# Kernel optimization log

Hardware: AMD Instinct MI355X
Metric: run time of the kernel (lower is better)

Reference implementation:

```python
import jax, jax.numpy as jnp
import numpy as np

L = 18                      # tree depth, N = 2**L - 1 nodes (complete binary tree)
N = 2**L - 1               # 262143
D = 128                     # embedding dim
V = 100000                  # vocab size of the single data type
E = 8                       # edge_count


def setup_inputs() -> dict:
    key = jax.random.key(0)
    ks = jax.random.split(key, 8)
    data = jax.random.randint(ks[0], (N,), 0, V)
    edges = jax.random.randint(ks[1], (N,), 0, E)
    data_vecs = jax.random.normal(ks[2], (V, D), dtype=jnp.float32) * 0.1
    # torch uses torch.rand (U[0,1)); scaled for numerical stability over 18 levels
    data_W = jax.random.uniform(ks[3], (D, D), dtype=jnp.float32) * 0.1
    data_b = jax.random.uniform(ks[4], (D,), dtype=jnp.float32) * 0.1
    edge_W = jax.random.uniform(ks[5], (E, D, D), dtype=jnp.float32) * (2.0 / D)
    edge_b = jax.random.uniform(ks[6], (E, D), dtype=jnp.float32) * 0.1
    score_W = jax.random.uniform(ks[7], (D, 1), dtype=jnp.float32)
    return {"data": data, "edges": edges, "data_vecs": data_vecs,
            "data_W": data_W, "data_b": data_b, "edge_W": edge_W,
            "edge_b": edge_b, "score_W": score_W}


def reference(data, edges, data_vecs, data_W, data_b, edge_W, edge_b, score_W):
    # per-node leaf term: addmm(data_bias, data_vecs[data], data_W)  -> [N, D]
    raw = data_vecs[data] @ data_W + data_b
    ret = raw    # value returned to the parent (leaves: unclamped)
    emb = raw    # stored embedding (internal nodes: pre-clamp h)
    # bottom-up over levels; level l occupies indices [2**l - 1, 2**(l+1) - 1)
    for l in reversed(range(L - 1)):
        p0, npar = 2**l - 1, 2**l
        c0, M = 2**(l + 1) - 1, 2**(l + 1)
        child_ret = ret[c0:c0 + M]              # [M, D], siblings adjacent
        eids = edges[c0:c0 + M]                 # [M]
        # edge-weighted child transform: child @ edge_W[e] + edge_b[e]
        contrib = edge_b[eids]
        for e in range(E):                      # small static edge loop
            contrib = contrib + jnp.where((eids == e)[:, None], child_ret, 0.0) @ edge_W[e]
        # sum the two children of each parent, then (leaf + children) / (nc + 1)
        contrib = contrib.reshape(npar, 2, D).sum(axis=1)
        h = (raw[p0:p0 + npar] + contrib) / 3.0
        emb = emb.at[p0:p0 + npar].set(h)
        ret = ret.at[p0:p0 + npar].set(jnp.maximum(h, 0.0))
    scores = (emb @ score_W)[:, 0]              # [N]
    return scores


if __name__ == "__main__":
    out = reference(**setup_inputs())
    print(out.shape, out.dtype)
```

## Files before the change

kernel.cpp:

```cpp
#include <hip/hip_runtime.h>

#define D 128
#define NLVL 17
#define TS 128
#define LVLPAD 1024
#define LDSTR 136
#define LEAF_BLKS 1032
#define CHUNK 2048
#define CNT_BLKS 128

typedef float  floatx4 __attribute__((ext_vector_type(4)));
typedef short  shortx8 __attribute__((ext_vector_type(8)));

__device__ __forceinline__ unsigned short f2bf(float f) {
    unsigned u = __float_as_uint(f);
    u += 0x7FFFu + ((u >> 16) & 1u);
    return (unsigned short)(u >> 16);
}
__device__ __forceinline__ float bf2f(unsigned short h) {
    return __uint_as_float(((unsigned)h) << 16);
}
__device__ __forceinline__ int lvl_base_dev(int l) { return ((2 << l) - 2) + LVLPAD * l; }

__global__ __launch_bounds__(256) void prep_kernel(
    const float* __restrict__ dW, const float* __restrict__ db,
    const float* __restrict__ eW, const float* __restrict__ eb,
    const float* __restrict__ sWs, const float* __restrict__ vecs,
    const int* __restrict__ edges,
    unsigned short* __restrict__ ewt, unsigned short* __restrict__ cwt,
    unsigned short* __restrict__ dwt, float* __restrict__ dcomp,
    float* __restrict__ sv, float* __restrict__ s0, int* __restrict__ ctr,
    int* __restrict__ gcnt128, int Nn,
    unsigned short* __restrict__ vbf, int n4)
{
    __shared__ float smem[8448];
    const int b = blockIdx.x, t = threadIdx.x;
    if (b < 32) {
        float* w_s = smem;
        float* cs  = smem + 4096;
        const int e = b >> 2, cc = b & 3;
        for (int i = t; i < D * 8; i += 256) {
            const int k = i >> 3, j4 = i & 7;
            ((float4*)w_s)[i] = ((const float4*)eW)[((size_t)e * D + k) * 32 + cc * 8 + j4];
        }
        __syncthreads();
        const int r2 = t >> 1, h = t & 1;
        float4 acc[4];
        #pragma unroll
        for (int m = 0; m < 4; m++) acc[m] = make_float4(0.f, 0.f, 0.f, 0.f);
        for (int k = 0; k < D; k++) {
            const float a = dW[(size_t)r2 * D + k];
            #pragma unroll
            for (int m = 0; m < 4; m++) {
                const float4 w4 = ((const float4*)w_s)[k * 8 + h * 4 + m];
                acc[m].x += a * w4.x; acc[m].y += a * w4.y; acc[m].z += a * w4.z; acc[m].w += a * w4.w;
            }
        }
        #pragma unroll
        for (int m = 0; m < 4; m++) {
            cs[r2 * 33 + h * 16 + m * 4 + 0] = acc[m].x;
            cs[r2 * 33 + h * 16 + m * 4 + 1] = acc[m].y;
            cs[r2 * 33 + h * 16 + m * 4 + 2] = acc[m].z;
            cs[r2 * 33 + h * 16 + m * 4 + 3] = acc[m].w;
        }
        __syncthreads();
        {
            const int nn = t >> 3, kseg = t & 7, k0 = kseg * 16;
            unsigned ow[8];
            #pragma unroll
            for (int i2 = 0; i2 < 8; i2++) {
                const unsigned short lo = f2bf(cs[(k0 + 2 * i2) * 33 + nn]);
                const unsigned short hi = f2bf(cs[(k0 + 2 * i2 + 1) * 33 + nn]);
                ow[i2] = (unsigned)lo | ((unsigned)hi << 16);
            }
            uint4* dstp = (uint4*)(cwt + (size_t)e * D * D + (size_t)(cc * 32 + nn) * D + k0);
            dstp[0] = make_uint4(ow[0], ow[1], ow[2], ow[3]);
            dstp[1] = make_uint4(ow[4], ow[5], ow[6], ow[7]);
        }
        if (t < 32) {
            float a2 = 0.f;
            for (int k = 0; k < D; k++) a2 += db[k] * w_s[k * 32 + t];
            dcomp[e * D + cc * 32 + t] = a2 + eb[e * D + cc * 32 + t];
        }
    } else if (b < 41) {
        float* lds = smem;
        const int bb = b - 32;
        const float* src = (bb < 8) ? (eW + (size_t)bb * D * D) : dW;
        unsigned short* dst = (bb < 8) ? (ewt + (size_t)bb * D * D) : dwt;
        for (int half = 0; half < 2; half++) {
            __syncthreads();
            for (int i = t; i < 64 * D / 4; i += 256) {
                float4 v = ((const float4*)src)[half * (64 * D / 4) + i];
                const int k = (i * 4) >> 7, n = (i * 4) & 127;
                lds[k * 129 + n]     = v.x;
                lds[k * 129 + n + 1] = v.y;
                lds[k * 129 + n + 2] = v.z;
                lds[k * 129 + n + 3] = v.w;
            }
            __syncthreads();
            const int n = t >> 1, hh = t & 1;
            for (int kk = 0; kk < 32; kk++) {
                const int k = hh * 32 + kk;
                dst[(size_t)n * D + half * 64 + k] = f2bf(lds[k * 129 + n]);
            }
        }
    } else if (b == 41) {
        float* red = smem;
        if (t < 32) ctr[t] = 0;
        if (t < D) {
            float acc = 0.f;
            for (int j = 0; j < D; j++) acc += dW[(size_t)t * D + j] * sWs[j];
            sv[t] = acc;
        }
        red[t] = (t < D) ? db[t] * sWs[t] : 0.f;
        __syncthreads();
        for (int s = 128; s > 0; s >>= 1) { if (t < s) red[t] += red[t + s]; __syncthreads(); }
        if (t == 0) s0[0] = red[0];
    } else if (b < 42 + CNT_BLKS) {
        int* lc = (int*)smem;
        if (t < 32) lc[t] = 0;
        __syncthreads();
        for (int c = 16383 + (b - 42) * 256 + t; c < Nn; c += CNT_BLKS * 256) {
            const int e = edges[c];
            const int p = (c - 1) >> 1;
            const int l = 31 - __clz(p + 1);
            atomicAdd(&lc[(l - 13) * 8 + e], 1);
        }
        __syncthreads();
        if (t < 32) gcnt128[(b - 42) * 32 + t] = lc[t];
    } else {
        for (int i = (b - 42 - CNT_BLKS) * 256 + t; i < n4; i += (gridDim.x - 42 - CNT_BLKS) * 256) {
            const float4 v = ((const float4*)vecs)[i];
            uint2 o;
            o.x = (unsigned)f2bf(v.x) | ((unsigned)f2bf(v.y) << 16);
            o.y = (unsigned)f2bf(v.z) | ((unsigned)f2bf(v.w) << 16);
            ((uint2*)vbf)[i] = o;
        }
    }
}

__global__ __launch_bounds__(256) void place_kernel(
    const int* __restrict__ edges, const int* __restrict__ gcnt128,
    int* __restrict__ gstart, int* __restrict__ glim,
    int* __restrict__ ctr, int* __restrict__ perm, int Nn)
{
    __shared__ unsigned char key_s[CHUNK];
    __shared__ int part[256];
    __shared__ int tot[32];
    __shared__ int lcnt[32], lbase[32];
    __shared__ int gs_s[4 * 9], gl_s[32];
    const int t = threadIdx.x;
    {
        const int k = t & 31, bs = t >> 5;
        int s = 0;
        for (int bb = bs; bb < CNT_BLKS; bb += 8) s += gcnt128[bb * 32 + k];
        part[t] = s;
    }
    if (t < 32) lcnt[t] = 0;
    __syncthreads();
    if (t < 32) {
        int tt = 0;
        #pragma unroll
        for (int i = 0; i < 8; i++) tt += part[t + 32 * i];
        tot[t] = tt;
    }
    __syncthreads();
    if (t == 0) {
        for (int li = 0; li < 4; li++) {
            int acc = 0;
            for (int e = 0; e < 8; e++) {
                gs_s[li * 9 + e] = acc;
                gl_s[li * 8 + e] = acc + tot[li * 8 + e];
                acc = (acc + tot[li * 8 + e] + (TS - 1)) & ~(TS - 1);
            }
            gs_s[li * 9 + 8] = acc;
        }
    }
    __syncthreads();
    if (blockIdx.x == 0 && t < 36) {
        gstart[13 * 9 + t] = gs_s[t];
        if (t < 32) glim[13 * 8 + t] = gl_s[t];
    }
    const int base = 16383 + blockIdx.x * CHUNK;
    for (int i = t; i < CHUNK; i += 256) {
        const int c = base + i;
        if (c < Nn) {
            const int e = edges[c];
            const int p = (c - 1) >> 1;
            const int l = 31 - __clz(p + 1);
            const int kk = (l - 13) * 8 + e;
            key_s[i] = (unsigned char)kk;
            atomicAdd(&lcnt[kk], 1);
        } else key_s[i] = 255;
    }
    __syncthreads();
    if (t < 32) {
        const int n = lcnt[t];
        lbase[t] = n ? atomicAdd(&ctr[t], n) : 0;
        lcnt[t] = 0;
    }
    __syncthreads();
    for (int i = t; i < CHUNK; i += 256) {
        const int c = base + i;
        if (c >= Nn) continue;
        const int kk = key_s[i];
        if (kk == 255) continue;
        const int off = atomicAdd(&lcnt[kk], 1);
        const int l = (kk >> 3) + 13, e = kk & 7;
        const int pos = gs_s[(l - 13) * 9 + e] + lbase[kk] + off;
        perm[lvl_base_dev(l) + pos] = c;
    }
}

__global__ __launch_bounds__(256, 4) void leaf_embed_kernel(
    unsigned short* __restrict__ X,
    const unsigned short* __restrict__ vbf,
    const int* __restrict__ data,
    const int* __restrict__ perm,
    const int* __restrict__ gstart9,
    const int* __restrict__ glim8,
    const unsigned short* __restrict__ cwt,
    const float* __restrict__ dcomp,
    const float* __restrict__ sv, const float* __restrict__ s0p,
    const unsigned short* __restrict__ dwt,
    const float* __restrict__ db,
    float* __restrict__ out,
    int NI, int lbase_leaf)
{
    __shared__ unsigned short a_s[TS * LDSTR];
    const int t = threadIdx.x;
    const bool is_leaf = (blockIdx.x < LEAF_BLKS);
    const int r = t >> 1, h = t & 1;

    int e = 0, c;
    const unsigned short* Wg;
    const float* bias;
    if (is_leaf) {
        const int ts = blockIdx.x * TS;
        if (ts >= gstart9[8]) return;
        #pragma unroll
        for (int j = 1; j < 8; j++) if (ts >= gstart9[j]) e = j;
        const int p = ts + r;
        c = (p < glim8[e]) ? perm[lbase_leaf + p] : -1;
        Wg = cwt + (size_t)e * D * D;
        bias = dcomp + (size_t)e * D;
    } else {
        const int node = (blockIdx.x - LEAF_BLKS) * TS + r;
        c = (node < NI) ? node : -1;
        Wg = dwt;
        bias = db;
    }

    {
        unsigned short* dst = a_s + r * LDSTR + h * 64;
        if (c >= 0) {
            const uint4* src = (const uint4*)(vbf + (size_t)data[c] * D + h * 64);
            if (is_leaf) {
                float sc = 0.f;
                #pragma unroll
                for (int j = 0; j < 8; j++) {
                    const uint4 v = src[j];
                    const unsigned* pv = (const unsigned*)&v;
                    #pragma unroll
                    for (int u = 0; u < 4; u++) {
                        const int n = h * 64 + j * 8 + u * 2;
                        sc += bf2f((unsigned short)pv[u]) * sv[n]
                            + bf2f((unsigned short)(pv[u] >> 16)) * sv[n + 1];
                    }
                    ((uint4*)dst)[j] = v;
                }
                sc += __shfl_xor(sc, 1, 64);
                if (h == 0) out[c] = sc + s0p[0];
            } else {
                #pragma unroll
                for (int j = 0; j < 8; j++) ((uint4*)dst)[j] = src[j];
            }
        } else {
            #pragma unroll
            for (int j = 0; j < 8; j++) ((uint4*)dst)[j] = make_uint4(0u, 0u, 0u, 0u);
        }
    }
    __syncthreads();

    const int lane = t & 63, wv = t >> 6;
    const int cq = lane & 15, q = lane >> 4;
    const floatx4 z4 = {0.f, 0.f, 0.f, 0.f};
    floatx4 acc[8][2];
    #pragma unroll
    for (int i = 0; i < 8; i++) { acc[i][0] = z4; acc[i][1] = z4; }
    #pragma unroll
    for (int ks = 0; ks < 4; ks++) {
        shortx8 bfr[2];
        #pragma unroll
        for (int nl = 0; nl < 2; nl++) {
            const int n = (wv * 2 + nl) * 16 + cq;
            bfr[nl] = *(const shortx8*)(Wg + (size_t)n * D + ks * 32 + q * 8);
        }
        #pragma unroll
        for (int mt = 0; mt < 8; mt++) {
            const shortx8 af = *(const shortx8*)(a_s + (mt * 16 + cq) * LDSTR + ks * 32 + q * 8);
            acc[mt][0] = __builtin_amdgcn_mfma_f32_16x16x32_bf16(af, bfr[0], acc[mt][0], 0, 0, 0);
            acc[mt][1] = __builtin_amdgcn_mfma_f32_16x16x32_bf16(af, bfr[1], acc[mt][1], 0, 0, 0);
        }
    }
    __syncthreads();
    #pragma unroll
    for (int nl = 0; nl < 2; nl++) {
        const int n = (wv * 2 + nl) * 16 + cq;
        const float bn = bias[n];
        #pragma unroll
        for (int mt = 0; mt < 8; mt++) {
            #pragma unroll
            for (int rg = 0; rg < 4; rg++) {
                const int m = mt * 16 + q * 4 + rg;
                a_s[m * LDSTR + n] = f2bf(acc[mt][nl][rg] + bn);
            }
        }
    }
    __syncthreads();
    if (c >= 0) {
        uint4* dst = (uint4*)(X + (size_t)c * D + h * 64);
        const uint4* srcl = (const uint4*)(a_s + r * LDSTR + h * 64);
        #pragma unroll
        for (int j = 0; j < 8; j++) dst[j] = srcl[j];
    }
}

__global__ __launch_bounds__(256, 4) void tree_gemm_kernel(
    unsigned short* __restrict__ X,
    const int* __restrict__ perm,
    const int* __restrict__ gstart9,
    const int* __restrict__ glim8,
    const unsigned short* __restrict__ ewt,
    const float* __restrict__ eb,
    const float* __restrict__ svec,
    float* __restrict__ out,
    int lbase)
{
    __shared__ unsigned short a_s[TS * LDSTR];
    const int t = threadIdx.x;
    const int ts = blockIdx.x * TS;
    if (ts >= gstart9[8]) return;
    int e = 0;
    #pragma unroll
    for (int j = 1; j < 8; j++) if (ts >= gstart9[j]) e = j;
    const int r = t >> 1, h = t & 1;
    const int p = ts + r;
    const int c = (p < glim8[e]) ? perm[lbase + p] : -1;
    const unsigned short* Wg = ewt + (size_t)e * D * D;

    {
        unsigned short* dst = a_s + r * LDSTR + h * 64;
        if (c >= 0) {
            const uint4* xr = (const uint4*)(X + (size_t)c * D + h * 64);
            const uint4* ya = (const uint4*)(X + (size_t)(2 * c + 1) * D + h * 64);
            const uint4* yb = (const uint4*)(X + (size_t)(2 * c + 2) * D + h * 64);
            const float inv3 = 1.0f / 3.0f;
            float sc = 0.f;
            #pragma unroll
            for (int j = 0; j < 8; j++) {
                uint4 ra = xr[j], rb = ya[j], rc = yb[j];
                const unsigned* pa = (const unsigned*)&ra;
                const unsigned* pb = (const unsigned*)&rb;
                const unsigned* pc = (const unsigned*)&rc;
                unsigned ou[4];
                #pragma unroll
                for (int u = 0; u < 4; u++) {
                    const float h0 = (bf2f((unsigned short)pa[u]) + bf2f((unsigned short)pb[u])
                                    + bf2f((unsigned short)pc[u])) * inv3;
                    const float h1 = (bf2f((unsigned short)(pa[u] >> 16)) + bf2f((unsigned short)(pb[u] >> 16))
                                    + bf2f((unsigned short)(pc[u] >> 16))) * inv3;
                    const int n = h * 64 + j * 8 + u * 2;
                    sc += h0 * svec[n] + h1 * svec[n + 1];
                    unsigned short q0 = f2bf(h0), q1 = f2bf(h1);
                    q0 = (q0 & 0x8000u) ? 0 : q0;
                    q1 = (q1 & 0x8000u) ? 0 : q1;
                    ou[u] = (unsigned)q0 | ((unsigned)q1 << 16);
                }
                ((uint4*)dst)[j] = make_uint4(ou[0], ou[1], ou[2], ou[3]);
            }
            sc += __shfl_xor(sc, 1, 64);
            if (h == 0) out[c] = sc;
        } else {
            #pragma unroll
            for (int j = 0; j < 8; j++) ((uint4*)dst)[j] = make_uint4(0u, 0u, 0u, 0u);
        }
    }
    __syncthreads();
    const int lane = t & 63, wv = t >> 6;
    const int cq = lane & 15, q = lane >> 4;
    const floatx4 z4 = {0.f, 0.f, 0.f, 0.f};
    floatx4 acc[8][2];
    #pragma unroll
    for (int i = 0; i < 8; i++) { acc[i][0] = z4; acc[i][1] = z4; }
    #pragma unroll
    for (int ks = 0; ks < 4; ks++) {
        shortx8 bfr[2];
        #pragma unroll
        for (int nl = 0; nl < 2; nl++) {
            const int n = (wv * 2 + nl) * 16 + cq;
            bfr[nl] = *(const shortx8*)(Wg + (size_t)n * D + ks * 32 + q * 8);
        }
        #pragma unroll
        for (int mt = 0; mt < 8; mt++) {
            const shortx8 af = *(const shortx8*)(a_s + (mt * 16 + cq) * LDSTR + ks * 32 + q * 8);
            acc[mt][0] = __builtin_amdgcn_mfma_f32_16x16x32_bf16(af, bfr[0], acc[mt][0], 0, 0, 0);
            acc[mt][1] = __builtin_amdgcn_mfma_f32_16x16x32_bf16(af, bfr[1], acc[mt][1], 0, 0, 0);
        }
    }
    __syncthreads();
    #pragma unroll
    for (int nl = 0; nl < 2; nl++) {
        const int n = (wv * 2 + nl) * 16 + cq;
        const float bn = eb[(size_t)e * D + n];
        #pragma unroll
        for (int mt = 0; mt < 8; mt++) {
            #pragma unroll
            for (int rg = 0; rg < 4; rg++) {
                const int m = mt * 16 + q * 4 + rg;
                a_s[m * LDSTR + n] = f2bf(acc[mt][nl][rg] + bn);
            }
        }
    }
    __syncthreads();
    if (c >= 0) {
        uint4* dst = (uint4*)(X + (size_t)c * D + h * 64);
        const uint4* srcl = (const uint4*)(a_s + r * LDSTR + h * 64);
        #pragma unroll
        for (int j = 0; j < 8; j++) dst[j] = srcl[j];
    }
}

__global__ __launch_bounds__(256) void sub_kernel(
    unsigned short* __restrict__ X,
    const float* __restrict__ eW,
    const float* __restrict__ eb,
    const int* __restrict__ edges,
    const float* __restrict__ sW,
    float* __restrict__ out,
    int rbase, int nlev)
{
    __shared__ __align__(16) float xbuf[4][D];
    const int t = threadIdx.x, wv = t >> 6, lane = t & 63;
    const int u = rbase + blockIdx.x;
    const int j2 = lane * 2;
    const float inv3 = 1.0f / 3.0f;

    for (int lev = nlev - 1; lev >= 0; lev--) {
        const int first = ((u + 1) << lev) - 1;
        const int cnt = 1 << lev;
        for (int i = wv; i < cnt; i += 4) {
            const int n = first + i;
            const unsigned ra = *(const unsigned*)(X + (size_t)n * D + j2);
            const unsigned rb = *(const unsigned*)(X + (size_t)(2 * n + 1) * D + j2);
            const unsigned rc = *(const unsigned*)(X + (size_t)(2 * n + 2) * D + j2);
            const float h0 = (bf2f((unsigned short)ra) + bf2f((unsigned short)rb)
                            + bf2f((unsigned short)rc)) * inv3;
            const float h1 = (bf2f((unsigned short)(ra >> 16)) + bf2f((unsigned short)(rb >> 16))
                            + bf2f((unsigned short)(rc >> 16))) * inv3;
            float sc = h0 * sW[j2] + h1 * sW[j2 + 1];
            #pragma unroll
            for (int o = 32; o > 0; o >>= 1) sc += __shfl_xor(sc, o, 64);
            if (lane == 0) out[n] = sc;
            if (n == 0) continue;
            float2 x2 = make_float2(fmaxf(h0, 0.f), fmaxf(h1, 0.f));
            *(float2*)(xbuf[wv] + j2) = x2;
            const int e = edges[n];
            const float* W = eW + (size_t)e * D * D;
            float y0 = 0.f, y1 = 0.f;
            #pragma unroll 8
            for (int k4 = 0; k4 < 32; k4++) {
                const float4 xk = *(const float4*)(xbuf[wv] + k4 * 4);
                const float2 w0 = *(const float2*)(W + (size_t)(k4 * 4 + 0) * D + j2);
                const float2 w1 = *(const float2*)(W + (size_t)(k4 * 4 + 1) * D + j2);
                const float2 w2 = *(const float2*)(W + (size_t)(k4 * 4 + 2) * D + j2);
                const float2 w3 = *(const float2*)(W + (size_t)(k4 * 4 + 3) * D + j2);
                y0 += xk.x * w0.x + xk.y * w1.x + xk.z * w2.x + xk.w * w3.x;
                y1 += xk.x * w0.y + xk.y * w1.y + xk.z * w2.y + xk.w * w3.y;
            }
            y0 += eb[e * D + j2];
            y1 += eb[e * D + j2 + 1];
            const unsigned o = (unsigned)f2bf(y0) | ((unsigned)f2bf(y1) << 16);
            *(unsigned*)(X + (size_t)n * D + j2) = o;
        }
        __syncthreads();
    }
}

extern "C" void kernel_launch(void* const* d_in, const int* in_sizes, int n_in,
                              void* d_out, int out_size, void* d_ws, size_t ws_size,
                              hipStream_t stream) {
    const int*   data      = (const int*)d_in[0];
    const int*   edges     = (const int*)d_in[1];
    const float* data_vecs = (const float*)d_in[2];
    const float* data_W    = (const float*)d_in[3];
    const float* data_b    = (const float*)d_in[4];
    const float* edge_W    = (const float*)d_in[5];
    const float* edge_b    = (const float*)d_in[6];
    const float* score_W   = (const float*)d_in[7];
    float* out = (float*)d_out;

    const int Nn = in_sizes[0];
    const int NI = Nn >> 1;
    const int VD = in_sizes[2];
    const int PERM_TOTAL = (Nn - 1) + LVLPAD * NLVL;

    char* w = (char*)d_ws;
    size_t off = 0;
    unsigned short* X = (unsigned short*)(w + off); off += (size_t)Nn * D * 2;
    int* perm = (int*)(w + off);  off += (size_t)PERM_TOTAL * 4;
    off = (off + 255) & ~(size_t)255;
    int* gstart  = (int*)(w + off); off += NLVL * 9 * 4;
    int* glim    = (int*)(w + off); off += NLVL * 8 * 4;
    int* gcnt128 = (int*)(w + off); off += CNT_BLKS * 32 * 4;
    int* ctr     = (int*)(w + off); off += 32 * 4;
    off = (off + 255) & ~(size_t)255;
    float* dcomp = (float*)(w + off); off += 8 * D * 4;
    float* sv    = (float*)(w + off); off += D * 4;
    float* s0    = (float*)(w + off); off += 256;
    off = (off + 255) & ~(size_t)255;
    unsigned short* ewt = (unsigned short*)(w + off); off += (size_t)8 * D * D * 2;
    unsigned short* cwt = (unsigned short*)(w + off); off += (size_t)8 * D * D * 2;
    unsigned short* dwt = (unsigned short*)(w + off); off += (size_t)D * D * 2;
    off = (off + 255) & ~(size_t)255;
    unsigned short* vbf = (unsigned short*)(w + off); off += (size_t)VD * 2;

    prep_kernel<<<42 + CNT_BLKS + 1024, 256, 0, stream>>>(
        data_W, data_b, edge_W, edge_b, score_W, data_vecs, edges,
        ewt, cwt, dwt, dcomp, sv, s0, ctr, gcnt128, Nn, vbf, VD / 4);

    const int place_blks = (Nn - 16383 + CHUNK - 1) / CHUNK;
    place_kernel<<<place_blks, 256, 0, stream>>>(edges, gcnt128, gstart, glim, ctr, perm, Nn);

    {
        const int embed_blks = (NI + TS - 1) / TS;
        const int lbase_leaf = ((2 << 16) - 2) + LVLPAD * 16;
        leaf_embed_kernel<<<LEAF_BLKS + embed_blks, 256, 0, stream>>>(
            X, vbf, data, perm, gstart + 16 * 9, glim + 16 * 8,
            cwt, dcomp, sv, s0, dwt, data_b, out, NI, lbase_leaf);
    }

    for (int l = 15; l >= 13; l--) {
        const int M = 2 << l;
        const int lbase = ((2 << l) - 2) + LVLPAD * l;
        tree_gemm_kernel<<<M / TS + 8, 256, 0, stream>>>(
            X, perm, gstart + l * 9, glim + l * 8, ewt, edge_b, score_W, out, lbase);
    }

    sub_kernel<<<2048, 256, 0, stream>>>(X, edge_W, edge_b, edges, score_W, out, 2047, 3);
    sub_kernel<<<128, 256, 0, stream>>>(X, edge_W, edge_b, edges, score_W, out, 127, 4);
    sub_kernel<<<8, 256, 0, stream>>>(X, edge_W, edge_b, edges, score_W, out, 7, 4);
    sub_kernel<<<1, 256, 0, stream>>>(X, edge_W, edge_b, edges, score_W, out, 0, 3);
}
```

Baseline: 336.0 us.

## Extend edge-grouped MFMA tree GEMM down to levels 10-12, drop 3-level subtree kernel

Extends the edge-sorted permutation (count and place kernels) to cover parent levels 10 through 15 instead of 13 through 15, widening the bin count from 32 to 56. The grouped tree_gemm kernel now also handles levels 12, 11 and 10, one launch per level, replacing the sub_kernel launch that processed three levels per subtree with 2048 blocks. This moves more work onto the matrix-core GEMM path. In exchange it adds three more launches with padded, small per-edge groups and a longer counting and placement pass.

```diff
diff --git a/kernel.cpp b/kernel.cpp
--- a/kernel.cpp
+++ b/kernel.cpp
@@ -8,6 +8,9 @@
 #define LEAF_BLKS 1032
 #define CHUNK 2048
 #define CNT_BLKS 128
+#define PLVL0 10
+#define CBASE 2047
+#define NBINS 56
 
 typedef float  floatx4 __attribute__((ext_vector_type(4)));
 typedef short  shortx8 __attribute__((ext_vector_type(8)));
@@ -106,7 +109,7 @@
         }
     } else if (b == 41) {
         float* red = smem;
-        if (t < 32) ctr[t] = 0;
+        if (t < NBINS) ctr[t] = 0;
         if (t < D) {
             float acc = 0.f;
             for (int j = 0; j < D; j++) acc += dW[(size_t)t * D + j] * sWs[j];
@@ -118,16 +121,16 @@
         if (t == 0) s0[0] = red[0];
     } else if (b < 42 + CNT_BLKS) {
         int* lc = (int*)smem;
-        if (t < 32) lc[t] = 0;
+        if (t < NBINS) lc[t] = 0;
         __syncthreads();
-        for (int c = 16383 + (b - 42) * 256 + t; c < Nn; c += CNT_BLKS * 256) {
+        for (int c = CBASE + (b - 42) * 256 + t; c < Nn; c += CNT_BLKS * 256) {
             const int e = edges[c];
             const int p = (c - 1) >> 1;
             const int l = 31 - __clz(p + 1);
-            atomicAdd(&lc[(l - 13) * 8 + e], 1);
+            atomicAdd(&lc[(l - PLVL0) * 8 + e], 1);
         }
         __syncthreads();
-        if (t < 32) gcnt128[(b - 42) * 32 + t] = lc[t];
+        if (t < NBINS) gcnt128[(b - 42) * NBINS + t] = lc[t];
     } else {
         for (int i = (b - 42 - CNT_BLKS) * 256 + t; i < n4; i += (gridDim.x - 42 - CNT_BLKS) * 256) {
             const float4 v = ((const float4*)vecs)[i];
@@ -146,27 +149,24 @@
 {
     __shared__ unsigned char key_s[CHUNK];
     __shared__ int part[256];
-    __shared__ int tot[32];
-    __shared__ int lcnt[32], lbase[32];
-    __shared__ int gs_s[4 * 9], gl_s[32];
+    __shared__ int tot[NBINS];
+    __shared__ int lcnt[NBINS], lbase[NBINS];
+    __shared__ int gs_s[7 * 9], gl_s[7 * 8];
     const int t = threadIdx.x;
     {
-        const int k = t & 31, bs = t >> 5;
+        const int k = t & 63, bs = t >> 6;
         int s = 0;
-        for (int bb = bs; bb < CNT_BLKS; bb += 8) s += gcnt128[bb * 32 + k];
+        if (k < NBINS)
+            for (int bb = bs; bb < CNT_BLKS; bb += 4) s += gcnt128[bb * NBINS + k];
         part[t] = s;
     }
-    if (t < 32) lcnt[t] = 0;
-    __syncthreads();
-    if (t < 32) {
-        int tt = 0;
-        #pragma unroll
-        for (int i = 0; i < 8; i++) tt += part[t + 32 * i];
-        tot[t] = tt;
-    }
+    if (t < NBINS) lcnt[t] = 0;
+    __syncthreads();
+    if (t < NBINS)
+        tot[t] = part[t] + part[t + 64] + part[t + 128] + part[t + 192];
     __syncthreads();
     if (t == 0) {
-        for (int li = 0; li < 4; li++) {
+        for (int li = 0; li < 7; li++) {
             int acc = 0;
             for (int e = 0; e < 8; e++) {
                 gs_s[li * 9 + e] = acc;
@@ -177,24 +177,24 @@
         }
     }
     __syncthreads();
-    if (blockIdx.x == 0 && t < 36) {
-        gstart[13 * 9 + t] = gs_s[t];
-        if (t < 32) glim[13 * 8 + t] = gl_s[t];
-    }
-    const int base = 16383 + blockIdx.x * CHUNK;
+    if (blockIdx.x == 0) {
+        if (t < 63) gstart[PLVL0 * 9 + t] = gs_s[t];
+        if (t < NBINS) glim[PLVL0 * 8 + t] = gl_s[t];
+    }
+    const int base = CBASE + blockIdx.x * CHUNK;
     for (int i = t; i < CHUNK; i += 256) {
         const int c = base + i;
         if (c < Nn) {
             const int e = edges[c];
             const int p = (c - 1) >> 1;
             const int l = 31 - __clz(p + 1);
-            const int kk = (l - 13) * 8 + e;
+            const int kk = (l - PLVL0) * 8 + e;
             key_s[i] = (unsigned char)kk;
             atomicAdd(&lcnt[kk], 1);
         } else key_s[i] = 255;
     }
     __syncthreads();
-    if (t < 32) {
+    if (t < NBINS) {
         const int n = lcnt[t];
         lbase[t] = n ? atomicAdd(&ctr[t], n) : 0;
         lcnt[t] = 0;
@@ -206,8 +206,8 @@
         const int kk = key_s[i];
         if (kk == 255) continue;
         const int off = atomicAdd(&lcnt[kk], 1);
-        const int l = (kk >> 3) + 13, e = kk & 7;
-        const int pos = gs_s[(l - 13) * 9 + e] + lbase[kk] + off;
+        const int l = (kk >> 3) + PLVL0, e = kk & 7;
+        const int pos = gs_s[(l - PLVL0) * 9 + e] + lbase[kk] + off;
         perm[lvl_base_dev(l) + pos] = c;
     }
 }
@@ -512,8 +512,8 @@
     off = (off + 255) & ~(size_t)255;
     int* gstart  = (int*)(w + off); off += NLVL * 9 * 4;
     int* glim    = (int*)(w + off); off += NLVL * 8 * 4;
-    int* gcnt128 = (int*)(w + off); off += CNT_BLKS * 32 * 4;
-    int* ctr     = (int*)(w + off); off += 32 * 4;
+    int* gcnt128 = (int*)(w + off); off += CNT_BLKS * 64 * 4;
+    int* ctr     = (int*)(w + off); off += 64 * 4;
     off = (off + 255) & ~(size_t)255;
     float* dcomp = (float*)(w + off); off += 8 * D * 4;
     float* sv    = (float*)(w + off); off += D * 4;
@@ -529,7 +529,7 @@
         data_W, data_b, edge_W, edge_b, score_W, data_vecs, edges,
         ewt, cwt, dwt, dcomp, sv, s0, ctr, gcnt128, Nn, vbf, VD / 4);
 
-    const int place_blks = (Nn - 16383 + CHUNK - 1) / CHUNK;
+    const int place_blks = (Nn - CBASE + CHUNK - 1) / CHUNK;
     place_kernel<<<place_blks, 256, 0, stream>>>(edges, gcnt128, gstart, glim, ctr, perm, Nn);
 
     {
@@ -540,14 +540,13 @@
             cwt, dcomp, sv, s0, dwt, data_b, out, NI, lbase_leaf);
     }
 
-    for (int l = 15; l >= 13; l--) {
+    for (int l = 15; l >= PLVL0; l--) {
         const int M = 2 << l;
         const int lbase = ((2 << l) - 2) + LVLPAD * l;
         tree_gemm_kernel<<<M / TS + 8, 256, 0, stream>>>(
             X, perm, gstart + l * 9, glim + l * 8, ewt, edge_b, score_W, out, lbase);
     }
 
-    sub_kernel<<<2048, 256, 0, stream>>>(X, edge_W, edge_b, edges, score_W, out, 2047, 3);
     sub_kernel<<<128, 256, 0, stream>>>(X, edge_W, edge_b, edges, score_W, out, 127, 4);
     sub_kernel<<<8, 256, 0, stream>>>(X, edge_W, edge_b, edges, score_W, out, 7, 4);
     sub_kernel<<<1, 256, 0, stream>>>(X, edge_W, edge_b, edges, score_W, out, 0, 3);
```

Result: faster. 313.8 us (-6.6%).
